# Performance work log

Hardware: AMD Instinct MI355X
Metric: run time of the kernel (lower is better)

Reference implementation:

```python
import jax, jax.numpy as jnp
import numpy as np

B, S, D, H = 2, 2048, 1024, 16
DK = D // H  # 64


def setup_inputs() -> dict:
    key = jax.random.key(0)
    ks = jax.random.split(key, 8)
    q = jax.random.normal(ks[0], (B, S, D), dtype=jnp.float32)
    k = jax.random.normal(ks[1], (B, S, D), dtype=jnp.float32)
    v = jax.random.normal(ks[2], (B, S, D), dtype=jnp.float32)
    mask = jax.random.randint(ks[3], (B, 1, S, S), 0, 2, dtype=jnp.int32)
    scale = 1.0 / np.sqrt(D)
    Wq = jax.random.normal(ks[4], (D, D), dtype=jnp.float32) * scale
    Wk = jax.random.normal(ks[5], (D, D), dtype=jnp.float32) * scale
    Wv = jax.random.normal(ks[6], (D, D), dtype=jnp.float32) * scale
    Wo = jax.random.normal(ks[7], (D, D), dtype=jnp.float32) * scale
    return {"q": q, "k": k, "v": v, "mask": mask,
            "Wq": Wq, "Wk": Wk, "Wv": Wv, "Wo": Wo}


def reference(q, k, v, mask, Wq, Wk, Wv, Wo):
    # Linear projections (torch nn.Linear: x @ W.T, no bias)
    qh = (q @ Wq.T).reshape(B, S, H, DK).transpose(0, 2, 1, 3)  # [B,H,S,DK]
    kh = (k @ Wk.T).reshape(B, S, H, DK).transpose(0, 2, 1, 3)
    vh = (v @ Wv.T).reshape(B, S, H, DK).transpose(0, 2, 1, 3)
    # Scaled dot-product attention with mask fill of -1e9 where mask == 0
    scores = jnp.einsum('bhqd,bhkd->bhqk', qh, kh) / jnp.sqrt(jnp.float32(DK))
    scores = jnp.where(mask == 0, jnp.float32(-1e9), scores)
    attn = jax.nn.softmax(scores, axis=-1)
    ctx = jnp.einsum('bhqk,bhkd->bhqd', attn, vh)  # [B,H,S,DK]
    ctx = ctx.transpose(0, 2, 1, 3).reshape(B, S, D)
    return ctx @ Wo.T
```

## Files before the change

### kernel.cpp

```cpp
#include <hip/hip_runtime.h>

using u16    = unsigned short;
using u32    = unsigned int;
using f32x4  = __attribute__((ext_vector_type(4))) float;
using f32x16 = __attribute__((ext_vector_type(16))) float;
using bf16x8 = __attribute__((ext_vector_type(8))) __bf16;
using u16x4  = __attribute__((ext_vector_type(4))) u16;
using u16x8  = __attribute__((ext_vector_type(8))) u16;
using u32x2  = __attribute__((ext_vector_type(2))) u32;
using u32x4  = __attribute__((ext_vector_type(4))) u32;
using i32x4  = __attribute__((ext_vector_type(4))) int;


__device__ __forceinline__ u16 f2bf(float f) {
  union { __bf16 b; u16 u; } c; c.b = (__bf16)f; return c.u;
}

typedef __attribute__((address_space(1))) const void GVoid;
typedef __attribute__((address_space(3))) void LVoid;

__device__ __forceinline__ void gload_lds16(const void* g, void* l) {
  __builtin_amdgcn_global_load_lds((GVoid*)g, (LVoid*)l, 16, 0, 0);
}

__global__ void cvt_w(const float* __restrict__ a, const float* __restrict__ b,
                      const float* __restrict__ c, const float* __restrict__ dd,
                      u16* __restrict__ oa, u16* __restrict__ ob,
                      u16* __restrict__ oc, u16* __restrict__ od) {
  int y = blockIdx.y;
  const float* s = (y == 0) ? a : (y == 1) ? b : (y == 2) ? c : dd;
  u16* d = (y == 0) ? oa : (y == 1) ? ob : (y == 2) ? oc : od;
  int i = blockIdx.x * 256 + threadIdx.x;
  f32x4 v = ((const f32x4*)s)[i];
  u16x4 r;
#pragma unroll
  for (int j = 0; j < 4; ++j) r[j] = f2bf(v[j]);
  ((u16x4*)d)[i] = r;
}

__global__ void pack_mask(const int* __restrict__ m, u32* __restrict__ mp) {
  int tid = blockIdx.x * 256 + threadIdx.x;
  int q = tid & 2047, kt = (tid >> 11) & 31, b = tid >> 16;
  const i32x4* src = (const i32x4*)(m + ((size_t)(b * 2048 + q)) * 2048 + kt * 64);
  u32 w0 = 0, w1 = 0;
#pragma unroll
  for (int j = 0; j < 8; ++j) {
    i32x4 a = src[j], c = src[j + 8];
#pragma unroll
    for (int e = 0; e < 4; ++e) {
      w0 |= (a[e] != 0 ? 1u : 0u) << (j * 4 + e);
      w1 |= (c[e] != 0 ? 1u : 0u) << (j * 4 + e);
    }
  }
  ((u32x2*)mp)[((size_t)(b * 32 + kt)) * 2048 + q] = u32x2{w0, w1};
}

__global__ __launch_bounds__(256, 2) void gemm_qkv(const float* __restrict__ Aq,
                                                   const float* __restrict__ Ak,
                                                   const float* __restrict__ Av,
                                                   const u16* __restrict__ Wb,
                                                   u16* __restrict__ out) {
  __shared__ alignas(16) char lds[49152];
  const int t = threadIdx.x;
  const int lane = t & 63, wid = t >> 6;
  const int g = lane >> 4, r16 = lane & 15;
  const int wm = wid >> 1, wn = wid & 1;
  const int m0 = blockIdx.x * 128, n0 = blockIdx.y * 128;
  const int z = blockIdx.z;

  const float* Axf = (z == 0) ? Aq : (z == 1) ? Ak : Av;
  const char* Ab = (const char*)Axf;
  const char* Bb = (const char*)(Wb + (size_t)z * 1048576);
  u16* op = out + (size_t)z * 4194304;
  const float qsc = (z == 0) ? 0.18033688011f : 1.0f;

  f32x4 acc[4][4] = {};

  for (int kk = 0; kk < 1024; kk += 64) {
#pragma unroll
    for (int i = 0; i < 8; ++i) {
      int ci = i * 256 + t;
      int row = ci >> 4;
      int pc = ci & 15;
      int lc = pc ^ (row & 15);
      gload_lds16(Ab + (size_t)(m0 + row) * 4096 + kk * 4 + lc * 16, lds + ci * 16);
    }
#pragma unroll
    for (int i = 0; i < 4; ++i) {
      int ci = i * 256 + t;
      int row = ci >> 3;
      int cbs = ((ci & 7) << 4) ^ ((row & 7) << 4);
      gload_lds16(Bb + (size_t)(n0 + row) * 2048 + kk * 2 + cbs, lds + 32768 + ci * 16);
    }
    __syncthreads();
#pragma unroll
    for (int kc = 0; kc < 2; ++kc) {
      bf16x8 af[4], bfr[4];
#pragma unroll
      for (int mf = 0; mf < 4; ++mf) {
        int row = wm * 64 + mf * 16 + r16;
        const char* arow = lds + row * 256;
        int x = row & 15;
        int lc0 = 8 * kc + 2 * g;
        f32x4 alo = *(const f32x4*)(arow + ((lc0 ^ x) * 16));
        f32x4 ahi = *(const f32x4*)(arow + (((lc0 + 1) ^ x) * 16));
        u16x8 pk;
#pragma unroll
        for (int j = 0; j < 4; ++j) { pk[j] = f2bf(alo[j]); pk[4 + j] = f2bf(ahi[j]); }
        af[mf] = __builtin_bit_cast(bf16x8, pk);
      }
#pragma unroll
      for (int nf = 0; nf < 4; ++nf) {
        int row = wn * 64 + nf * 16 + r16;
        bfr[nf] = *(const bf16x8*)(lds + 32768 + row * 128 +
                                   ((64 * kc + 16 * g) ^ ((row & 7) << 4)));
      }
#pragma unroll
      for (int mf = 0; mf < 4; ++mf)
#pragma unroll
        for (int nf = 0; nf < 4; ++nf)
          acc[mf][nf] = __builtin_amdgcn_mfma_f32_16x16x32_bf16(af[mf], bfr[nf], acc[mf][nf], 0, 0, 0);
    }
    __syncthreads();
  }

#pragma unroll
  for (int mf = 0; mf < 4; ++mf) {
#pragma unroll
    for (int nf = 0; nf < 4; ++nf) {
      int mb = m0 + wm * 64 + mf * 16 + 4 * g;
      int n = n0 + wn * 64 + nf * 16 + r16;
      if (z == 0) {
        int bb = mb >> 11, h = n >> 6, dk = n & 63;
#pragma unroll
        for (int r = 0; r < 4; ++r) {
          int s2 = (mb + r) & 2047;
          op[((size_t)(bb * 16 + h) * 2048 + s2) * 64 + dk] = f2bf(acc[mf][nf][r] * qsc);
        }
      } else if (z == 1) {
        int h = n >> 6, dk = n & 63;
#pragma unroll
        for (int r = 0; r < 4; ++r) {
          int m = mb + r;
          int bb = m >> 11, s2 = m & 2047;
          size_t off16 = ((((size_t)(bb * 16 + h) * 32 + (s2 >> 6)) * 2 + ((s2 >> 5) & 1)) * 8 +
                          (dk >> 3)) * 32 + (s2 & 31);
          op[off16 * 8 + (dk & 7)] = f2bf(acc[mf][nf][r]);
        }
      } else {
        int bb = mb >> 11, s2 = mb & 2047, h = n >> 6, d = n & 63;
        size_t off16 = ((((size_t)(bb * 16 + h) * 32 + (s2 >> 6)) * 8 + ((s2 & 63) >> 3)) * 2 +
                        (d >> 5)) * 32 + (d & 31);
        u16x4 pv;
#pragma unroll
        for (int r = 0; r < 4; ++r) pv[r] = f2bf(acc[mf][nf][r]);
        *(u16x4*)(op + off16 * 8 + (s2 & 7)) = pv;
      }
    }
  }
}

__global__ __launch_bounds__(256, 2) void gemm_out(const u16* __restrict__ X,
                                                   const u16* __restrict__ W,
                                                   float* __restrict__ out) {
  __shared__ alignas(16) char lds[32768];
  const int t = threadIdx.x;
  const int lane = t & 63, wid = t >> 6;
  const int g = lane >> 4, r16 = lane & 15;
  const int wm = wid >> 1, wn = wid & 1;
  const int m0 = blockIdx.x * 128, n0 = blockIdx.y * 128;
  const char* Ab = (const char*)X;
  const char* Bb = (const char*)W;

  f32x4 acc[4][4] = {};

  for (int kk = 0; kk < 1024; kk += 64) {
#pragma unroll
    for (int i = 0; i < 4; ++i) {
      int ci = i * 256 + t;
      int row = ci >> 3;
      int cbs = ((ci & 7) << 4) ^ ((row & 7) << 4);
      gload_lds16(Ab + (size_t)(m0 + row) * 2048 + kk * 2 + cbs, lds + ci * 16);
      gload_lds16(Bb + (size_t)(n0 + row) * 2048 + kk * 2 + cbs, lds + 16384 + ci * 16);
    }
    __syncthreads();
#pragma unroll
    for (int kc = 0; kc < 2; ++kc) {
      bf16x8 af[4], bfr[4];
#pragma unroll
      for (int mf = 0; mf < 4; ++mf) {
        int row = wm * 64 + mf * 16 + r16;
        af[mf] = *(const bf16x8*)(lds + row * 128 + ((64 * kc + 16 * g) ^ ((row & 7) << 4)));
      }
#pragma unroll
      for (int nf = 0; nf < 4; ++nf) {
        int row = wn * 64 + nf * 16 + r16;
        bfr[nf] = *(const bf16x8*)(lds + 16384 + row * 128 + ((64 * kc + 16 * g) ^ ((row & 7) << 4)));
      }
#pragma unroll
      for (int mf = 0; mf < 4; ++mf)
#pragma unroll
        for (int nf = 0; nf < 4; ++nf)
          acc[mf][nf] = __builtin_amdgcn_mfma_f32_16x16x32_bf16(af[mf], bfr[nf], acc[mf][nf], 0, 0, 0);
    }
    __syncthreads();
  }

#pragma unroll
  for (int mf = 0; mf < 4; ++mf)
#pragma unroll
    for (int nf = 0; nf < 4; ++nf) {
      int mb = m0 + wm * 64 + mf * 16 + 4 * g;
      int n = n0 + wn * 64 + nf * 16 + r16;
#pragma unroll
      for (int r = 0; r < 4; ++r) out[(size_t)(mb + r) * 1024 + n] = acc[mf][nf][r];
    }
}

struct KF { bf16x8 k0[4], k1[4]; };

__device__ __forceinline__ void loadK(KF& f, const char* p) {
#pragma unroll
  for (int c = 0; c < 4; ++c) {
    f.k0[c] = *(const bf16x8*)(p + c * 1024);
    f.k1[c] = *(const bf16x8*)(p + 4096 + c * 1024);
  }
}

__device__ __forceinline__ void half_pass(const bf16x8 (&qf)[4], const bf16x8 (&kh)[4],
                                          const char* vp0, const char* vp1, int ksbase,
                                          u32 wmask, float (&psx)[4],
                                          f32x16& o0, f32x16& o1) {
  bf16x8 va0 = *(const bf16x8*)(vp0 + (ksbase + 0) * 2048);
  bf16x8 va1 = *(const bf16x8*)(vp0 + (ksbase + 1) * 2048);
  bf16x8 vb0 = *(const bf16x8*)(vp1 + (ksbase + 0) * 2048);
  bf16x8 vb1 = *(const bf16x8*)(vp1 + (ksbase + 1) * 2048);

  f32x16 s = {};
#pragma unroll
  for (int c = 0; c < 4; ++c)
    s = __builtin_amdgcn_mfma_f32_32x32x16_bf16(kh[c], qf[c], s, 0, 0, 0);

#pragma unroll
  for (int r = 0; r < 16; ++r) {
    const int bit = (r & 3) + 8 * (r >> 2);
    float p = __builtin_amdgcn_exp2f(s[r]);
    int sm;
    asm("v_bfe_i32 %0, %1, %2, 1" : "=v"(sm) : "v"(wmask), "i"(bit));
    p = __uint_as_float(__float_as_uint(p) & (u32)sm);
    s[r] = p;
    psx[r & 3] += p;
  }

  u32 w[8];
#pragma unroll
  for (int ss = 0; ss < 2; ++ss) {
    u32 A0, B0, A1, B1;
    asm("v_cvt_pk_bf16_f32 %0, %1, %2" : "=v"(A0) : "v"(s[8*ss+0]), "v"(s[8*ss+1]));
    asm("v_cvt_pk_bf16_f32 %0, %1, %2" : "=v"(B0) : "v"(s[8*ss+2]), "v"(s[8*ss+3]));
    asm("v_cvt_pk_bf16_f32 %0, %1, %2" : "=v"(A1) : "v"(s[8*ss+4]), "v"(s[8*ss+5]));
    asm("v_cvt_pk_bf16_f32 %0, %1, %2" : "=v"(B1) : "v"(s[8*ss+6]), "v"(s[8*ss+7]));
    asm("v_permlane32_swap_b32 %0, %1" : "+v"(A0), "+v"(A1));
    asm("v_permlane32_swap_b32 %0, %1" : "+v"(B0), "+v"(B1));
    w[4*ss+0] = A0; w[4*ss+1] = B0; w[4*ss+2] = A1; w[4*ss+3] = B1;
  }

  bf16x8 pa0 = __builtin_bit_cast(bf16x8, u32x4{w[0], w[1], w[2], w[3]});
  bf16x8 pa1 = __builtin_bit_cast(bf16x8, u32x4{w[4], w[5], w[6], w[7]});
  o0 = __builtin_amdgcn_mfma_f32_32x32x16_bf16(pa0, va0, o0, 0, 0, 0);
  o1 = __builtin_amdgcn_mfma_f32_32x32x16_bf16(pa0, vb0, o1, 0, 0, 0);
  o0 = __builtin_amdgcn_mfma_f32_32x32x16_bf16(pa1, va1, o0, 0, 0, 0);
  o1 = __builtin_amdgcn_mfma_f32_32x32x16_bf16(pa1, vb1, o1, 0, 0, 0);
}

__device__ __forceinline__ void attn_body(const bf16x8 (&qf)[4], KF& cur, KF& nxt,
                                          const char*& kp, const char*& vp0,
                                          const char*& vp1, const u32x2*& mptr,
                                          u32x2& mcur, int hi,
                                          f32x16& o0, f32x16& o1, float& l_run) {
  loadK(nxt, kp);
  u32x2 mnext = *mptr;
  kp += 8192; mptr += 2048;
  __builtin_amdgcn_sched_barrier(0);

  float psx[4] = {0.f, 0.f, 0.f, 0.f};
  half_pass(qf, cur.k0, vp0, vp1, 0, mcur.x >> (4 * hi), psx, o0, o1);
  half_pass(qf, cur.k1, vp0, vp1, 2, mcur.y >> (4 * hi), psx, o0, o1);
  l_run += (psx[0] + psx[1]) + (psx[2] + psx[3]);

  vp0 += 8192; vp1 += 8192;
  mcur = mnext;
}

__global__ __launch_bounds__(256, 3) void attn_kern(const u16* __restrict__ Qh,
                                                    const u16* __restrict__ Kh,
                                                    const u16* __restrict__ Vt,
                                                    const u32* __restrict__ mp,
                                                    u16* __restrict__ ctx) {
  __shared__ float cmb[2][32][64];
  __shared__ float cmbl[2][64];
  const int t = threadIdx.x;
  const int wid = t >> 6, lane = t & 63;
  const int qw = wid & 1, kh = wid >> 1;
  const int hi = lane >> 5, l31 = lane & 31;

  const int wg = (blockIdx.x & 7) * 128 + (blockIdx.x >> 3);
  const int qt = wg & 31, bh = wg >> 5;
  const int b = bh >> 4, h = bh & 15;

  const char* qbytes = (const char*)Qh;
  const int qbase = qt * 64 + qw * 32;
  const int qg = qbase + l31;

  bf16x8 qf[4];
#pragma unroll
  for (int c = 0; c < 4; ++c)
    qf[c] = *(const bf16x8*)(qbytes + ((size_t)bh * 2048 + qg) * 128 + 32 * c + 16 * hi);

  const char* kp  = (const char*)Kh + (size_t)bh * 262144 + (size_t)kh * 131072 + hi * 512 + l31 * 16;
  const char* vp0 = (const char*)Vt + (size_t)bh * 262144 + (size_t)kh * 131072 + hi * 1024 + l31 * 16;
  const char* vp1 = vp0 + 512;
  const u32x2* mptr = (const u32x2*)mp + (size_t)b * 65536 + (size_t)kh * 32768 + qg;

  f32x16 o0 = {}, o1 = {};
  float l_run = 0.f;

  KF A, B2;
  loadK(A, kp);
  kp += 8192;
  u32x2 mcur = *mptr;
  mptr += 2048;

#pragma unroll 1
  for (int it = 0; it < 8; ++it) {
    attn_body(qf, A, B2, kp, vp0, vp1, mptr, mcur, hi, o0, o1, l_run);
    attn_body(qf, B2, A, kp, vp0, vp1, mptr, mcur, hi, o0, o1, l_run);
  }

  l_run += __shfl_xor(l_run, 32, 64);

  if (kh) {
#pragma unroll
    for (int r = 0; r < 16; ++r) {
      cmb[qw][r][lane]      = o0[r];
      cmb[qw][16 + r][lane] = o1[r];
    }
    cmbl[qw][lane] = l_run;
  }
  __syncthreads();
  if (!kh) {
#pragma unroll
    for (int r = 0; r < 16; ++r) {
      o0[r] += cmb[qw][r][lane];
      o1[r] += cmb[qw][16 + r][lane];
    }
    l_run += cmbl[qw][lane];

    float rl = 1.f / l_run;
#pragma unroll
    for (int r = 0; r < 16; ++r) {
      float rv = __shfl(rl, (r & 3) + 8 * (r >> 2) + 4 * hi, 64);
      int q = qbase + (r & 3) + 8 * (r >> 2) + 4 * hi;
      size_t rowp = ((size_t)b * 2048 + q) * 1024 + h * 64 + l31;
      ctx[rowp]      = f2bf(o0[r] * rv);
      ctx[rowp + 32] = f2bf(o1[r] * rv);
    }
  }
}

extern "C" void kernel_launch(void* const* d_in, const int* in_sizes, int n_in,
                              void* d_out, int out_size, void* d_ws, size_t ws_size,
                              hipStream_t stream) {
  const float* q  = (const float*)d_in[0];
  const float* k  = (const float*)d_in[1];
  const float* v  = (const float*)d_in[2];
  const int* mask = (const int*)d_in[3];
  const float* Wq = (const float*)d_in[4];
  const float* Wk = (const float*)d_in[5];
  const float* Wv = (const float*)d_in[6];
  const float* Wo = (const float*)d_in[7];

  u16* ws = (u16*)d_ws;
  const size_t NX = (size_t)4096 * 1024;
  const size_t NW = (size_t)1024 * 1024;
  u16* Wqb = ws + 3 * NX;
  u16* Qh  = Wqb + 4 * NW;
  u16* ctx = Qh + 3 * NX;
  u32* mpk = (u32*)ws;

  cvt_w<<<dim3(1024, 4), 256, 0, stream>>>(Wq, Wk, Wv, Wo,
                                           Wqb, Wqb + NW, Wqb + 2 * NW, Wqb + 3 * NW);
  pack_mask<<<dim3(512), 256, 0, stream>>>(mask, mpk);
  gemm_qkv<<<dim3(32, 8, 3), 256, 0, stream>>>(q, k, v, Wqb, Qh);
  attn_kern<<<dim3(1024), 256, 0, stream>>>(Qh, Qh + NX, Qh + 2 * NX, mpk, ctx);
  gemm_out<<<dim3(32, 8), 256, 0, stream>>>(ctx, Wqb + 3 * NW, (float*)d_out);
}
```

Measured before the change: 143.8 us.

## Stage K/V tiles through double-buffered LDS with async global-to-LDS loads in attention

The attention kernel now loads each 64-key K and V tile cooperatively into a double-buffered LDS region using global_load_lds. Each tile is shared by both wave pairs, which read their halves from LDS, in place of every wave reading its own K and V directly from global memory into registers. Each iteration waits on vmcnt and uses two block barriers. This cuts register pressure and duplicate global traffic, but adds barrier synchronisation and LDS reads. Launch bounds are also swapped: attn goes from 3 to 2 waves per SIMD and gemm_qkv from 2 to 3.

```diff
diff --git a/kernel.cpp b/kernel.cpp
--- a/kernel.cpp
+++ b/kernel.cpp
@@ -55,7 +55,7 @@
   ((u32x2*)mp)[((size_t)(b * 32 + kt)) * 2048 + q] = u32x2{w0, w1};
 }
 
-__global__ __launch_bounds__(256, 2) void gemm_qkv(const float* __restrict__ Aq,
+__global__ __launch_bounds__(256, 3) void gemm_qkv(const float* __restrict__ Aq,
                                                    const float* __restrict__ Ak,
                                                    const float* __restrict__ Av,
                                                    const u16* __restrict__ Wb,
@@ -217,88 +217,12 @@
     }
 }
 
-struct KF { bf16x8 k0[4], k1[4]; };
-
-__device__ __forceinline__ void loadK(KF& f, const char* p) {
-#pragma unroll
-  for (int c = 0; c < 4; ++c) {
-    f.k0[c] = *(const bf16x8*)(p + c * 1024);
-    f.k1[c] = *(const bf16x8*)(p + 4096 + c * 1024);
-  }
-}
-
-__device__ __forceinline__ void half_pass(const bf16x8 (&qf)[4], const bf16x8 (&kh)[4],
-                                          const char* vp0, const char* vp1, int ksbase,
-                                          u32 wmask, float (&psx)[4],
-                                          f32x16& o0, f32x16& o1) {
-  bf16x8 va0 = *(const bf16x8*)(vp0 + (ksbase + 0) * 2048);
-  bf16x8 va1 = *(const bf16x8*)(vp0 + (ksbase + 1) * 2048);
-  bf16x8 vb0 = *(const bf16x8*)(vp1 + (ksbase + 0) * 2048);
-  bf16x8 vb1 = *(const bf16x8*)(vp1 + (ksbase + 1) * 2048);
-
-  f32x16 s = {};
-#pragma unroll
-  for (int c = 0; c < 4; ++c)
-    s = __builtin_amdgcn_mfma_f32_32x32x16_bf16(kh[c], qf[c], s, 0, 0, 0);
-
-#pragma unroll
-  for (int r = 0; r < 16; ++r) {
-    const int bit = (r & 3) + 8 * (r >> 2);
-    float p = __builtin_amdgcn_exp2f(s[r]);
-    int sm;
-    asm("v_bfe_i32 %0, %1, %2, 1" : "=v"(sm) : "v"(wmask), "i"(bit));
-    p = __uint_as_float(__float_as_uint(p) & (u32)sm);
-    s[r] = p;
-    psx[r & 3] += p;
-  }
-
-  u32 w[8];
-#pragma unroll
-  for (int ss = 0; ss < 2; ++ss) {
-    u32 A0, B0, A1, B1;
-    asm("v_cvt_pk_bf16_f32 %0, %1, %2" : "=v"(A0) : "v"(s[8*ss+0]), "v"(s[8*ss+1]));
-    asm("v_cvt_pk_bf16_f32 %0, %1, %2" : "=v"(B0) : "v"(s[8*ss+2]), "v"(s[8*ss+3]));
-    asm("v_cvt_pk_bf16_f32 %0, %1, %2" : "=v"(A1) : "v"(s[8*ss+4]), "v"(s[8*ss+5]));
-    asm("v_cvt_pk_bf16_f32 %0, %1, %2" : "=v"(B1) : "v"(s[8*ss+6]), "v"(s[8*ss+7]));
-    asm("v_permlane32_swap_b32 %0, %1" : "+v"(A0), "+v"(A1));
-    asm("v_permlane32_swap_b32 %0, %1" : "+v"(B0), "+v"(B1));
-    w[4*ss+0] = A0; w[4*ss+1] = B0; w[4*ss+2] = A1; w[4*ss+3] = B1;
-  }
-
-  bf16x8 pa0 = __builtin_bit_cast(bf16x8, u32x4{w[0], w[1], w[2], w[3]});
-  bf16x8 pa1 = __builtin_bit_cast(bf16x8, u32x4{w[4], w[5], w[6], w[7]});
-  o0 = __builtin_amdgcn_mfma_f32_32x32x16_bf16(pa0, va0, o0, 0, 0, 0);
-  o1 = __builtin_amdgcn_mfma_f32_32x32x16_bf16(pa0, vb0, o1, 0, 0, 0);
-  o0 = __builtin_amdgcn_mfma_f32_32x32x16_bf16(pa1, va1, o0, 0, 0, 0);
-  o1 = __builtin_amdgcn_mfma_f32_32x32x16_bf16(pa1, vb1, o1, 0, 0, 0);
-}
-
-__device__ __forceinline__ void attn_body(const bf16x8 (&qf)[4], KF& cur, KF& nxt,
-                                          const char*& kp, const char*& vp0,
-                                          const char*& vp1, const u32x2*& mptr,
-                                          u32x2& mcur, int hi,
-                                          f32x16& o0, f32x16& o1, float& l_run) {
-  loadK(nxt, kp);
-  u32x2 mnext = *mptr;
-  kp += 8192; mptr += 2048;
-  __builtin_amdgcn_sched_barrier(0);
-
-  float psx[4] = {0.f, 0.f, 0.f, 0.f};
-  half_pass(qf, cur.k0, vp0, vp1, 0, mcur.x >> (4 * hi), psx, o0, o1);
-  half_pass(qf, cur.k1, vp0, vp1, 2, mcur.y >> (4 * hi), psx, o0, o1);
-  l_run += (psx[0] + psx[1]) + (psx[2] + psx[3]);
-
-  vp0 += 8192; vp1 += 8192;
-  mcur = mnext;
-}
-
-__global__ __launch_bounds__(256, 3) void attn_kern(const u16* __restrict__ Qh,
+__global__ __launch_bounds__(256, 2) void attn_kern(const u16* __restrict__ Qh,
                                                     const u16* __restrict__ Kh,
                                                     const u16* __restrict__ Vt,
                                                     const u32* __restrict__ mp,
                                                     u16* __restrict__ ctx) {
-  __shared__ float cmb[2][32][64];
-  __shared__ float cmbl[2][64];
+  __shared__ alignas(16) char lds[32768];
   const int t = threadIdx.x;
   const int wid = t >> 6, lane = t & 63;
   const int qw = wid & 1, kh = wid >> 1;
@@ -317,44 +241,119 @@
   for (int c = 0; c < 4; ++c)
     qf[c] = *(const bf16x8*)(qbytes + ((size_t)bh * 2048 + qg) * 128 + 32 * c + 16 * hi);
 
-  const char* kp  = (const char*)Kh + (size_t)bh * 262144 + (size_t)kh * 131072 + hi * 512 + l31 * 16;
-  const char* vp0 = (const char*)Vt + (size_t)bh * 262144 + (size_t)kh * 131072 + hi * 1024 + l31 * 16;
-  const char* vp1 = vp0 + 512;
-  const u32x2* mptr = (const u32x2*)mp + (size_t)b * 65536 + (size_t)kh * 32768 + qg;
+  const char* ktile = (const char*)Kh + (size_t)bh * 262144;
+  const char* vtile = (const char*)Vt + (size_t)bh * 262144;
+  const u32x2* mptr = (const u32x2*)mp + (size_t)b * 65536 + qg;
 
   f32x16 o0 = {}, o1 = {};
   float l_run = 0.f;
 
-  KF A, B2;
-  loadK(A, kp);
-  kp += 8192;
+#define STAGE(BUF, KT)                                                          \
+  {                                                                             \
+    _Pragma("unroll") for (int i = 0; i < 2; ++i) {                             \
+      int ci = i * 256 + t;                                                     \
+      gload_lds16(ktile + (size_t)(KT) * 8192 + ci * 16,                        \
+                  lds + (BUF) * 16384 + ci * 16);                               \
+      gload_lds16(vtile + (size_t)(KT) * 8192 + ci * 16,                        \
+                  lds + (BUF) * 16384 + 8192 + ci * 16);                        \
+    }                                                                           \
+  }
+
+  STAGE(0, 0);
   u32x2 mcur = *mptr;
   mptr += 2048;
 
 #pragma unroll 1
-  for (int it = 0; it < 8; ++it) {
-    attn_body(qf, A, B2, kp, vp0, vp1, mptr, mcur, hi, o0, o1, l_run);
-    attn_body(qf, B2, A, kp, vp0, vp1, mptr, mcur, hi, o0, o1, l_run);
-  }
+  for (int kt = 0; kt < 32; ++kt) {
+    const char* cb = lds + (kt & 1) * 16384;
+    u32x2 mnext;
+    if (kt < 31) {
+      STAGE((kt + 1) & 1, kt + 1);
+      mnext = *mptr;
+      mptr += 2048;
+      asm volatile("s_waitcnt vmcnt(5)" ::: "memory");
+    } else {
+      mnext = mcur;
+      asm volatile("s_waitcnt vmcnt(0)" ::: "memory");
+    }
+    __builtin_amdgcn_s_barrier();
+    asm volatile("" ::: "memory");
+
+    bf16x8 kf[4];
+#pragma unroll
+    for (int c = 0; c < 4; ++c)
+      kf[c] = *(const bf16x8*)(cb + kh * 4096 + c * 1024 + hi * 512 + l31 * 16);
+
+    f32x16 s = {};
+#pragma unroll
+    for (int c = 0; c < 4; ++c)
+      s = __builtin_amdgcn_mfma_f32_32x32x16_bf16(kf[c], qf[c], s, 0, 0, 0);
+
+    u32 wm = (kh ? mcur.y : mcur.x) >> (4 * hi);
+    float ps = 0.f;
+#pragma unroll
+    for (int r = 0; r < 16; ++r) {
+      const int bit = (r & 3) + 8 * (r >> 2);
+      float p = __builtin_amdgcn_exp2f(s[r]);
+      int sm = ((int)(wm << (31 - bit))) >> 31;
+      p = __uint_as_float(__float_as_uint(p) & (u32)sm);
+      s[r] = p;
+      ps += p;
+    }
+    l_run += ps;
+
+    u32 w[8];
+#pragma unroll
+    for (int ss = 0; ss < 2; ++ss) {
+      u32 A0, B0, A1, B1;
+      asm("v_cvt_pk_bf16_f32 %0, %1, %2" : "=v"(A0) : "v"(s[8*ss+0]), "v"(s[8*ss+1]));
+      asm("v_cvt_pk_bf16_f32 %0, %1, %2" : "=v"(B0) : "v"(s[8*ss+2]), "v"(s[8*ss+3]));
+      asm("v_cvt_pk_bf16_f32 %0, %1, %2" : "=v"(A1) : "v"(s[8*ss+4]), "v"(s[8*ss+5]));
+      asm("v_cvt_pk_bf16_f32 %0, %1, %2" : "=v"(B1) : "v"(s[8*ss+6]), "v"(s[8*ss+7]));
+      asm("v_permlane32_swap_b32 %0, %1" : "+v"(A0), "+v"(A1));
+      asm("v_permlane32_swap_b32 %0, %1" : "+v"(B0), "+v"(B1));
+      w[4*ss+0] = A0; w[4*ss+1] = B0; w[4*ss+2] = A1; w[4*ss+3] = B1;
+    }
+
+#pragma unroll
+    for (int ss = 0; ss < 2; ++ss) {
+      bf16x8 pa = __builtin_bit_cast(bf16x8, u32x4{w[4*ss], w[4*ss+1], w[4*ss+2], w[4*ss+3]});
+      const char* vbase = cb + 8192 + (size_t)(4 * kh + 2 * ss + hi) * 1024 + l31 * 16;
+      bf16x8 v0 = *(const bf16x8*)(vbase);
+      bf16x8 v1 = *(const bf16x8*)(vbase + 512);
+      o0 = __builtin_amdgcn_mfma_f32_32x32x16_bf16(pa, v0, o0, 0, 0, 0);
+      o1 = __builtin_amdgcn_mfma_f32_32x32x16_bf16(pa, v1, o1, 0, 0, 0);
+    }
+
+    asm volatile("" ::: "memory");
+    __builtin_amdgcn_s_barrier();
+    asm volatile("" ::: "memory");
+    mcur = mnext;
+  }
+#undef STAGE
+
+  __syncthreads();
+  float* cmb  = (float*)lds;
+  float* cmbl = (float*)(lds + 16384);
 
   l_run += __shfl_xor(l_run, 32, 64);
 
   if (kh) {
 #pragma unroll
     for (int r = 0; r < 16; ++r) {
-      cmb[qw][r][lane]      = o0[r];
-      cmb[qw][16 + r][lane] = o1[r];
-    }
-    cmbl[qw][lane] = l_run;
+      cmb[(qw * 32 + r) * 64 + lane]      = o0[r];
+      cmb[(qw * 32 + 16 + r) * 64 + lane] = o1[r];
+    }
+    cmbl[qw * 64 + lane] = l_run;
   }
   __syncthreads();
   if (!kh) {
 #pragma unroll
     for (int r = 0; r < 16; ++r) {
-      o0[r] += cmb[qw][r][lane];
-      o1[r] += cmb[qw][16 + r][lane];
-    }
-    l_run += cmbl[qw][lane];
+      o0[r] += cmb[(qw * 32 + r) * 64 + lane];
+      o1[r] += cmb[(qw * 32 + 16 + r) * 64 + lane];
+    }
+    l_run += cmbl[qw * 64 + lane];
 
     float rl = 1.f / l_run;
 #pragma unroll
```

New measurement: 127.9 us. 11.1% less time.

## Interleave key split across waves and halve per-iteration K fragment registers

Applied to the files above, without the earlier changes.

The attention kernel's key range is now split between the two wave groups at 32-key granularity, interleaved, instead of giving each group a contiguous half. Each step loads a single 32-key K fragment and its matching V rows, cutting the double-buffered K registers in half, and the loop runs twice as many steps. The mask bit extract moves from inline v_bfe asm to shift arithmetic, and the QKV GEMM launch bound rises from 2 to 3 waves per SIMD, which may force register spills. The aim is lower register pressure and better latency hiding, at the cost of more loop overhead per key.

```diff
diff --git a/kernel.cpp b/kernel.cpp
--- a/kernel.cpp
+++ b/kernel.cpp
@@ -55,7 +55,7 @@
   ((u32x2*)mp)[((size_t)(b * 32 + kt)) * 2048 + q] = u32x2{w0, w1};
 }
 
-__global__ __launch_bounds__(256, 2) void gemm_qkv(const float* __restrict__ Aq,
+__global__ __launch_bounds__(256, 3) void gemm_qkv(const float* __restrict__ Aq,
                                                    const float* __restrict__ Ak,
                                                    const float* __restrict__ Av,
                                                    const u16* __restrict__ Wb,
@@ -217,40 +217,44 @@
     }
 }
 
-struct KF { bf16x8 k0[4], k1[4]; };
-
-__device__ __forceinline__ void loadK(KF& f, const char* p) {
-#pragma unroll
-  for (int c = 0; c < 4; ++c) {
-    f.k0[c] = *(const bf16x8*)(p + c * 1024);
-    f.k1[c] = *(const bf16x8*)(p + 4096 + c * 1024);
-  }
-}
-
-__device__ __forceinline__ void half_pass(const bf16x8 (&qf)[4], const bf16x8 (&kh)[4],
-                                          const char* vp0, const char* vp1, int ksbase,
-                                          u32 wmask, float (&psx)[4],
-                                          f32x16& o0, f32x16& o1) {
-  bf16x8 va0 = *(const bf16x8*)(vp0 + (ksbase + 0) * 2048);
-  bf16x8 va1 = *(const bf16x8*)(vp0 + (ksbase + 1) * 2048);
-  bf16x8 vb0 = *(const bf16x8*)(vp1 + (ksbase + 0) * 2048);
-  bf16x8 vb1 = *(const bf16x8*)(vp1 + (ksbase + 1) * 2048);
+struct KH { bf16x8 k[4]; };
+
+__device__ __forceinline__ void loadKh(KH& f, const char* p) {
+#pragma unroll
+  for (int c = 0; c < 4; ++c) f.k[c] = *(const bf16x8*)(p + c * 1024);
+}
+
+__device__ __forceinline__ void attn_body(const bf16x8 (&qf)[4], KH& cur, KH& nxt,
+                                          const char*& kp, const char*& vp,
+                                          const u32x2*& mptr, u32x2& mcur,
+                                          int kh, int hi,
+                                          f32x16& o0, f32x16& o1, float& l_run) {
+  bf16x8 v00 = *(const bf16x8*)(vp);
+  bf16x8 v01 = *(const bf16x8*)(vp + 512);
+  bf16x8 v10 = *(const bf16x8*)(vp + 2048);
+  bf16x8 v11 = *(const bf16x8*)(vp + 2560);
+  loadKh(nxt, kp);
+  u32x2 mnext = *mptr;
+  kp += 8192; vp += 8192; mptr += 2048;
+  __builtin_amdgcn_sched_barrier(0);
 
   f32x16 s = {};
 #pragma unroll
   for (int c = 0; c < 4; ++c)
-    s = __builtin_amdgcn_mfma_f32_32x32x16_bf16(kh[c], qf[c], s, 0, 0, 0);
-
+    s = __builtin_amdgcn_mfma_f32_32x32x16_bf16(cur.k[c], qf[c], s, 0, 0, 0);
+
+  u32 wm = (kh ? mcur.y : mcur.x) >> (4 * hi);
+  float ps = 0.f;
 #pragma unroll
   for (int r = 0; r < 16; ++r) {
     const int bit = (r & 3) + 8 * (r >> 2);
     float p = __builtin_amdgcn_exp2f(s[r]);
-    int sm;
-    asm("v_bfe_i32 %0, %1, %2, 1" : "=v"(sm) : "v"(wmask), "i"(bit));
+    int sm = ((int)(wm << (31 - bit))) >> 31;
     p = __uint_as_float(__float_as_uint(p) & (u32)sm);
     s[r] = p;
-    psx[r & 3] += p;
-  }
+    ps += p;
+  }
+  l_run += ps;
 
   u32 w[8];
 #pragma unroll
@@ -267,28 +271,10 @@
 
   bf16x8 pa0 = __builtin_bit_cast(bf16x8, u32x4{w[0], w[1], w[2], w[3]});
   bf16x8 pa1 = __builtin_bit_cast(bf16x8, u32x4{w[4], w[5], w[6], w[7]});
-  o0 = __builtin_amdgcn_mfma_f32_32x32x16_bf16(pa0, va0, o0, 0, 0, 0);
-  o1 = __builtin_amdgcn_mfma_f32_32x32x16_bf16(pa0, vb0, o1, 0, 0, 0);
-  o0 = __builtin_amdgcn_mfma_f32_32x32x16_bf16(pa1, va1, o0, 0, 0, 0);
-  o1 = __builtin_amdgcn_mfma_f32_32x32x16_bf16(pa1, vb1, o1, 0, 0, 0);
-}
-
-__device__ __forceinline__ void attn_body(const bf16x8 (&qf)[4], KF& cur, KF& nxt,
-                                          const char*& kp, const char*& vp0,
-                                          const char*& vp1, const u32x2*& mptr,
-                                          u32x2& mcur, int hi,
-                                          f32x16& o0, f32x16& o1, float& l_run) {
-  loadK(nxt, kp);
-  u32x2 mnext = *mptr;
-  kp += 8192; mptr += 2048;
-  __builtin_amdgcn_sched_barrier(0);
-
-  float psx[4] = {0.f, 0.f, 0.f, 0.f};
-  half_pass(qf, cur.k0, vp0, vp1, 0, mcur.x >> (4 * hi), psx, o0, o1);
-  half_pass(qf, cur.k1, vp0, vp1, 2, mcur.y >> (4 * hi), psx, o0, o1);
-  l_run += (psx[0] + psx[1]) + (psx[2] + psx[3]);
-
-  vp0 += 8192; vp1 += 8192;
+  o0 = __builtin_amdgcn_mfma_f32_32x32x16_bf16(pa0, v00, o0, 0, 0, 0);
+  o1 = __builtin_amdgcn_mfma_f32_32x32x16_bf16(pa0, v01, o1, 0, 0, 0);
+  o0 = __builtin_amdgcn_mfma_f32_32x32x16_bf16(pa1, v10, o0, 0, 0, 0);
+  o1 = __builtin_amdgcn_mfma_f32_32x32x16_bf16(pa1, v11, o1, 0, 0, 0);
   mcur = mnext;
 }
 
@@ -317,24 +303,23 @@
   for (int c = 0; c < 4; ++c)
     qf[c] = *(const bf16x8*)(qbytes + ((size_t)bh * 2048 + qg) * 128 + 32 * c + 16 * hi);
 
-  const char* kp  = (const char*)Kh + (size_t)bh * 262144 + (size_t)kh * 131072 + hi * 512 + l31 * 16;
-  const char* vp0 = (const char*)Vt + (size_t)bh * 262144 + (size_t)kh * 131072 + hi * 1024 + l31 * 16;
-  const char* vp1 = vp0 + 512;
-  const u32x2* mptr = (const u32x2*)mp + (size_t)b * 65536 + (size_t)kh * 32768 + qg;
+  const char* kp = (const char*)Kh + (size_t)bh * 262144 + kh * 4096 + hi * 512 + l31 * 16;
+  const char* vp = (const char*)Vt + (size_t)bh * 262144 + (size_t)(4 * kh + hi) * 1024 + l31 * 16;
+  const u32x2* mptr = (const u32x2*)mp + (size_t)b * 65536 + qg;
 
   f32x16 o0 = {}, o1 = {};
   float l_run = 0.f;
 
-  KF A, B2;
-  loadK(A, kp);
+  KH A, B2;
+  loadKh(A, kp);
   kp += 8192;
   u32x2 mcur = *mptr;
   mptr += 2048;
 
 #pragma unroll 1
-  for (int it = 0; it < 8; ++it) {
-    attn_body(qf, A, B2, kp, vp0, vp1, mptr, mcur, hi, o0, o1, l_run);
-    attn_body(qf, B2, A, kp, vp0, vp1, mptr, mcur, hi, o0, o1, l_run);
+  for (int it = 0; it < 16; ++it) {
+    attn_body(qf, A, B2, kp, vp, mptr, mcur, kh, hi, o0, o1, l_run);
+    attn_body(qf, B2, A, kp, vp, mptr, mcur, kh, hi, o0, o1, l_run);
   }
 
   l_run += __shfl_xor(l_run, 32, 64);
```

After: 126.1 us. 12.3% less time.
